# Kernel optimization log

Hardware: AMD Instinct MI355X
Metric: run time of the kernel (lower is better)

## Reference

```python
import jax, jax.numpy as jnp
from jax import lax
import numpy as np

B, C, H, W = 16, 32, 128, 128
R = 8      # region_num
OUT = 32   # out_channels (== in_channels, required by residual add)
K = 3      # kernel_size
PAD = 1    # self.kwargs padding for the correlation conv


def setup_inputs() -> dict:
    key = jax.random.key(0)
    ks = jax.random.split(key, 8)
    n = lambda k, s: jax.random.normal(k, s, dtype=jnp.float32) * 0.05
    return {
        "input": jax.random.normal(ks[0], (B, C, H, W), dtype=jnp.float32),
        "guide_input": jax.random.normal(ks[1], (B, C, H, W), dtype=jnp.float32),
        "w1": n(ks[2], (R * R, C)), "b1": jnp.zeros((R * R,), jnp.float32),
        "w2": n(ks[3], (R, C * OUT, R)), "b2": jnp.zeros((R * C * OUT,), jnp.float32),
        "w_spa": n(ks[4], (R, C)), "b_spa": jnp.zeros((R,), jnp.float32),
        "w_spec": n(ks[5], (R, C)), "b_spec": jnp.zeros((R,), jnp.float32),
        "w_f": n(ks[6], (OUT, 2 * C, 3, 3)), "b_f": jnp.zeros((OUT,), jnp.float32),
    }


def adaptive_avg_pool2d(x, k):
    # torch AdaptiveAvgPool2d bin edges: start=floor(i*H/k), end=ceil((i+1)*H/k)
    Hh, Ww = x.shape[-2], x.shape[-1]
    rows = []
    for i in range(k):
        hs, he = (i * Hh) // k, -(-((i + 1) * Hh) // k)
        cols = []
        for j in range(k):
            ws, we = (j * Ww) // k, -(-((j + 1) * Ww) // k)
            cols.append(x[..., hs:he, ws:we].mean(axis=(-2, -1)))
        rows.append(jnp.stack(cols, axis=-1))
    return jnp.stack(rows, axis=-2)  # [..., k, k]


def asign_index(kernel, guide):
    # kernel: [B, R, OUT, H, W]; guide: [B, R, H, W]
    mask = jax.nn.one_hot(jnp.argmax(guide, axis=1), guide.shape[1], axis=1,
                          dtype=kernel.dtype)  # [B, R, H, W]
    return jnp.sum(kernel * mask[:, :, None], axis=1)  # [B, OUT, H, W]


def reference(input, guide_input, w1, b1, w2, b2, w_spa, b_spa, w_spec, b_spec, w_f, b_f):
    # --- dynamic kernel generation (conv_kernel Sequential) ---
    pooled = adaptive_avg_pool2d(input, K)                                    # [B, C, K, K]
    g = jax.nn.sigmoid(jnp.einsum('bckl,oc->bokl', pooled, w1) + b1[None, :, None, None])  # [B, R*R, K, K]
    g = g.reshape(B, R, R, K, K)
    # grouped 1x1 conv (groups=R): per group in=R, out=C*OUT
    kern = jnp.einsum('brikl,roi->brokl', g, w2).reshape(B, R * C * OUT, K, K)
    kern = kern + b2[None, :, None, None]
    kern = kern.reshape(B, R * OUT, C, K, K)

    # --- correlation: per-sample conv with its own generated kernels (xcorr_fast) ---
    corr = jax.vmap(lambda xi, ki: lax.conv_general_dilated(
        xi[None], ki, (1, 1), [(PAD, PAD), (PAD, PAD)])[0])(input, kern)      # [B, R*OUT, H, W]
    corr = corr.reshape(B, R, OUT, H, W)

    # --- guide features (SpecDynConv / SpecClassifier modeled as 1x1 convs C->R) ---
    gf_spa = jnp.einsum('bchw,rc->brhw', guide_input, w_spa) + b_spa[None, :, None, None]
    gf_spec = jnp.einsum('bchw,rc->brhw', guide_input, w_spec) + b_spec[None, :, None, None]

    # --- argmax one-hot mask select + region-sum ---
    out_spa = asign_index(corr, gf_spa)    # [B, OUT, H, W]
    out_spec = asign_index(corr, gf_spec)  # [B, OUT, H, W]

    # --- fusion conv 3x3 + residual ---
    fused = lax.conv_general_dilated(jnp.concatenate([out_spa, out_spec], axis=1),
                                     w_f, (1, 1), [(1, 1), (1, 1)])
    fused = fused + b_f[None, :, None, None]
    return fused + input
```

## Files before the change

### kernel.cpp

```cpp
#include <hip/hip_runtime.h>
#include <hip/hip_bf16.h>
#include <math.h>

#define Bn 16
#define Cn 32
#define Hn 128
#define Wn 128
#define HW (Hn*Wn)
#define Rn 8
#define OUTn 32
#define PW 130

#define OFF_POOLED 0u
#define OFF_G      18432u
#define OFF_KERNA  55296u
#define OFF_WFA    2414592u
#define OFF_RSEL   2451456u
#define OFF_INTP   3500032u
#define OFF_CATP   20805632u

typedef __attribute__((ext_vector_type(8))) short short8;
typedef __attribute__((ext_vector_type(4))) float floatx4;

static __device__ __forceinline__ unsigned short f2b(float f) {
  __hip_bfloat16 h = __float2bfloat16(f);
  return *reinterpret_cast<unsigned short*>(&h);
}


__global__ __launch_bounds__(64) void pool_kernel(const float* __restrict__ in,
                                                  float* __restrict__ pooled) {
  const int blk = blockIdx.x;
  const int bin = blk % 9, bc = blk / 9;
  const int bi = bin / 3, bj = bin % 3;
  const int s0[3] = {0, 42, 85};
  const int e0[3] = {43, 86, 128};
  const int rs = s0[bi], re = e0[bi];
  const int cs = s0[bj], ce = e0[bj];
  const int n = (re - rs) * (ce - cs);
  const float* img = in + (size_t)bc * HW;
  float acc = 0.f;
  for (int y = rs; y < re; ++y)
    for (int x = cs + (int)threadIdx.x; x < ce; x += 64)
      acc += img[y * Wn + x];
  #pragma unroll
  for (int off = 32; off > 0; off >>= 1) acc += __shfl_down(acc, off, 64);
  if (threadIdx.x == 0) pooled[bc * 9 + bin] = acc / (float)n;
}

__global__ void g_kernel(const float* __restrict__ pooled, const float* __restrict__ w1,
                         const float* __restrict__ b1, float* __restrict__ g) {
  const int idx = blockIdx.x * 256 + threadIdx.x;
  if (idx >= Bn * 64 * 9) return;
  const int bin = idx % 9;
  const int o = (idx / 9) % 64;
  const int b = idx / (9 * 64);
  float acc = b1[o];
  #pragma unroll
  for (int c = 0; c < Cn; ++c)
    acc = fmaf(pooled[(b * Cn + c) * 9 + bin], w1[o * Cn + c], acc);
  g[idx] = 1.f / (1.f + expf(-acc));
}

__global__ void kern_kernel(const float* __restrict__ g, const float* __restrict__ w2,
                            const float* __restrict__ b2, short* __restrict__ kernA) {
  const int idx = blockIdx.x * 256 + threadIdx.x;
  if (idx >= Bn * 8 * 9 * 1024) return;
  const int j  = idx & 7;
  const int m  = (idx >> 3) & 15;
  const int kg = (idx >> 7) & 3;
  const int h  = (idx >> 9) & 1;
  const int t  = (idx >> 10) % 9;
  const int br = idx / 9216;
  const int r = br & 7, b = br >> 3;
  const int c = kg * 8 + j;
  const int u = h * 16 + m;
  const int jidx = u * 32 + c;
  float acc = b2[r * 1024 + jidx];
  #pragma unroll
  for (int i = 0; i < 8; ++i)
    acc = fmaf(g[(b * 64 + r * 8 + i) * 9 + t], w2[(r * 1024 + jidx) * 8 + i], acc);
  kernA[idx] = (short)f2b(acc);
}

__global__ void wf_kernel(const float* __restrict__ w_f, short* __restrict__ wfA) {
  int idx = blockIdx.x * 256 + threadIdx.x;
  if (idx >= 18432) return;
  const int j  = idx & 7;
  const int m  = (idx >> 3) & 15;
  const int kg = (idx >> 7) & 3;
  const int h  = (idx >> 9) & 1;
  const int kb = idx >> 10;
  const int tap = kb >> 1, ch = kb & 1;
  const int ci = ch * 32 + kg * 8 + j;
  const int o = h * 16 + m;
  wfA[idx] = (short)f2b(w_f[(o * 64 + ci) * 9 + tap]);
}


__global__ void halo_kernel(uint4* __restrict__ inTp, uint4* __restrict__ catp) {
  const int idx = blockIdx.x * 256 + threadIdx.x;
  if (idx >= Bn * 520) return;
  const int b = idx / 520, i = idx % 520;
  int y, x;
  if (i < 130)      { y = 0;       x = i; }
  else if (i < 260) { y = 129;     x = i - 130; }
  else if (i < 390) { y = i - 260; x = 0; }
  else              { y = i - 390; x = 129; }
  const size_t pp = (size_t)(b * PW + y) * PW + x;
  const uint4 z = make_uint4(0u, 0u, 0u, 0u);
  #pragma unroll
  for (int q = 0; q < 4; ++q) inTp[pp * 4 + q] = z;
  #pragma unroll
  for (int q = 0; q < 8; ++q) catp[pp * 8 + q] = z;
}


__global__ __launch_bounds__(256) void tr_kernel(const float* __restrict__ in,
                                                 uint4* __restrict__ inTp) {
  __shared__ float lds[32][65];
  const int blk = blockIdx.x;
  const int b = blk >> 8;
  const int p0 = (blk & 255) * 64;
  const int tid = threadIdx.x;
  const int pl = tid & 63;
  const int c0 = tid >> 6;
  #pragma unroll
  for (int cc = 0; cc < 8; ++cc) {
    const int c = cc * 4 + c0;
    lds[c][pl] = in[(size_t)(b * 32 + c) * HW + p0 + pl];
  }
  __syncthreads();
  const int pw = tid >> 2;
  const int cg = (tid & 3) * 8;
  unsigned int w0 = (unsigned)f2b(lds[cg + 0][pw]) | ((unsigned)f2b(lds[cg + 1][pw]) << 16);
  unsigned int w1 = (unsigned)f2b(lds[cg + 2][pw]) | ((unsigned)f2b(lds[cg + 3][pw]) << 16);
  unsigned int w2 = (unsigned)f2b(lds[cg + 4][pw]) | ((unsigned)f2b(lds[cg + 5][pw]) << 16);
  unsigned int w3 = (unsigned)f2b(lds[cg + 6][pw]) | ((unsigned)f2b(lds[cg + 7][pw]) << 16);
  const int p = p0 + pw;
  const int y = p >> 7, x = p & 127;
  const size_t pp = (size_t)(b * PW + y + 1) * PW + (x + 1);
  inTp[pp * 4 + (tid & 3)] = make_uint4(w0, w1, w2, w3);
}


__global__ void rsel_kernel(const float* __restrict__ guide,
                            const float* __restrict__ w_spa, const float* __restrict__ b_spa,
                            const float* __restrict__ w_spec, const float* __restrict__ b_spec,
                            int* __restrict__ rsel) {
  const int idx = blockIdx.x * 256 + threadIdx.x;
  const int b = idx >> 14;
  const int p = idx & (HW - 1);
  float gv[Cn];
  const float* gp = guide + (size_t)b * Cn * HW + p;
  #pragma unroll
  for (int c = 0; c < Cn; ++c) gv[c] = gp[c * HW];
  int best1 = 0, best2 = 0;
  float bv1 = -1e30f, bv2 = -1e30f;
  for (int r = 0; r < Rn; ++r) {
    float v1 = b_spa[r], v2 = b_spec[r];
    #pragma unroll
    for (int c = 0; c < Cn; ++c) {
      v1 = fmaf(gv[c], w_spa[r * Cn + c], v1);
      v2 = fmaf(gv[c], w_spec[r * Cn + c], v2);
    }
    if (v1 > bv1) { bv1 = v1; best1 = r; }
    if (v2 > bv2) { bv2 = v2; best2 = r; }
  }
  rsel[idx] = best1 | (best2 << 8);
}


__global__ __launch_bounds__(256) void stageB_kernel(
    const char* __restrict__ inTp, const short* __restrict__ kernA,
    const int* __restrict__ rsel, char* __restrict__ catp) {
  const int id = blockIdx.x;
  const int chunk = id & 7, r = (id >> 3) & 7, b = id >> 6;
  const int pbase = chunk * 2048;
  __shared__ int lcount;
  __shared__ unsigned short list[4096];
  const int tid = threadIdx.x;
  if (tid == 0) lcount = 0;
  __syncthreads();
  const int* rs = rsel + b * HW + pbase;
  for (int i = tid; i < 2048; i += 256) {
    int v = rs[i];
    if ((v & 255) == r) { int k = atomicAdd(&lcount, 1); list[k] = (unsigned short)i; }
    if ((v >> 8) == r)  { int k = atomicAdd(&lcount, 1); list[k] = (unsigned short)(i | 2048); }
  }
  __syncthreads();
  const int cnt = lcount;
  const int lane = tid & 63, wid = tid >> 6;
  const int l15 = lane & 15, kg = lane >> 4;

  short8 aw[18];
  {
    const short* kb = kernA + (size_t)(b * 8 + r) * 18 * 512;
    #pragma unroll
    for (int f = 0; f < 18; ++f)
      aw[f] = *(const short8*)(kb + f * 512 + kg * 128 + l15 * 8);
  }

  for (int g = wid; g * 16 < cnt; g += 4) {
    const int e16 = g * 16 + l15;
    const bool ev = e16 < cnt;
    const int ent = list[ev ? e16 : 0];
    const int p = pbase + (ent & 2047);
    const int which = ent >> 11;
    const int y = p >> 7, x = p & 127;
    const size_t pp = (size_t)(b * PW + y + 1) * PW + (x + 1);
    const char* base = inTp + pp * 64 + kg * 16;
    floatx4 acc0 = {0.f, 0.f, 0.f, 0.f}, acc1 = {0.f, 0.f, 0.f, 0.f};
    #pragma unroll
    for (int t = 0; t < 9; ++t) {
      const int dy = t / 3 - 1, dx = t % 3 - 1;
      const short8 bx = *(const short8*)(base + (dy * PW + dx) * 64);
      acc0 = __builtin_amdgcn_mfma_f32_16x16x32_bf16(aw[t * 2 + 0], bx, acc0, 0, 0, 0);
      acc1 = __builtin_amdgcn_mfma_f32_16x16x32_bf16(aw[t * 2 + 1], bx, acc1, 0, 0, 0);
    }
    if (ev) {
      char* op = catp + pp * 128 + which * 64 + kg * 8;
      uint2 v0, v1;
      v0.x = (unsigned)f2b(acc0[0]) | ((unsigned)f2b(acc0[1]) << 16);
      v0.y = (unsigned)f2b(acc0[2]) | ((unsigned)f2b(acc0[3]) << 16);
      v1.x = (unsigned)f2b(acc1[0]) | ((unsigned)f2b(acc1[1]) << 16);
      v1.y = (unsigned)f2b(acc1[2]) | ((unsigned)f2b(acc1[3]) << 16);
      *(uint2*)op = v0;
      *(uint2*)(op + 32) = v1;
    }
  }
}


__global__ __launch_bounds__(256, 4) void stageC_kernel(
    const char* __restrict__ catp, const short* __restrict__ wfA,
    const float* __restrict__ b_f, const float* __restrict__ in,
    float* __restrict__ out) {
  __shared__ short lwf[18432];
  const int tid = threadIdx.x;
  {
    const uint4* src = (const uint4*)wfA;
    uint4* dst = (uint4*)lwf;
    #pragma unroll
    for (int i = 0; i < 9; ++i)
      dst[i * 256 + tid] = src[i * 256 + tid];
  }
  __syncthreads();
  const int id = (blockIdx.x & 7) * 128 + (blockIdx.x >> 3);
  const int b = id >> 6, seg = id & 63;
  const int lane = tid & 63, wid = tid >> 6;
  const int l15 = lane & 15, kg = lane >> 4;
  const int pix = seg * 256 + wid * 64 + l15;

  const char* bq[4];
  #pragma unroll
  for (int q = 0; q < 4; ++q) {
    const int p = pix + q * 16;
    const int y = p >> 7, x = p & 127;
    bq[q] = catp + ((size_t)(b * PW + y + 1) * PW + (x + 1)) * 128 + kg * 16;
  }
  floatx4 acc[2][4] = {};
  #pragma unroll
  for (int kb = 0; kb < 18; ++kb) {
    const int tap = kb >> 1, ch = kb & 1;
    const int dy = tap / 3 - 1, dx = tap % 3 - 1;
    const int goff = (dy * PW + dx) * 128 + ch * 64;
    const short8 a0 = *(const short8*)&lwf[(kb * 2 + 0) * 512 + kg * 128 + l15 * 8];
    const short8 a1 = *(const short8*)&lwf[(kb * 2 + 1) * 512 + kg * 128 + l15 * 8];
    #pragma unroll
    for (int q = 0; q < 4; ++q) {
      const short8 bx = *(const short8*)(bq[q] + goff);
      acc[0][q] = __builtin_amdgcn_mfma_f32_16x16x32_bf16(a0, bx, acc[0][q], 0, 0, 0);
      acc[1][q] = __builtin_amdgcn_mfma_f32_16x16x32_bf16(a1, bx, acc[1][q], 0, 0, 0);
    }
  }
  #pragma unroll
  for (int h = 0; h < 2; ++h) {
    const int o0 = h * 16 + kg * 4;
    #pragma unroll
    for (int q = 0; q < 4; ++q) {
      const int p = pix + q * 16;
      #pragma unroll
      for (int reg = 0; reg < 4; ++reg) {
        const size_t oi = (size_t)(b * 32 + o0 + reg) * HW + p;
        out[oi] = acc[h][q][reg] + b_f[o0 + reg] + in[oi];
      }
    }
  }
}


extern "C" void kernel_launch(void* const* d_in, const int* in_sizes, int n_in,
                              void* d_out, int out_size, void* d_ws, size_t ws_size,
                              hipStream_t stream) {
  const float* input  = (const float*)d_in[0];
  const float* guide  = (const float*)d_in[1];
  const float* w1     = (const float*)d_in[2];
  const float* b1     = (const float*)d_in[3];
  const float* w2     = (const float*)d_in[4];
  const float* b2     = (const float*)d_in[5];
  const float* w_spa  = (const float*)d_in[6];
  const float* b_spa  = (const float*)d_in[7];
  const float* w_spec = (const float*)d_in[8];
  const float* b_spec = (const float*)d_in[9];
  const float* w_f    = (const float*)d_in[10];
  const float* b_f    = (const float*)d_in[11];
  float* out = (float*)d_out;

  char* ws = (char*)d_ws;
  float* pooled = (float*)(ws + OFF_POOLED);
  float* g      = (float*)(ws + OFF_G);
  short* kernA  = (short*)(ws + OFF_KERNA);
  short* wfA    = (short*)(ws + OFF_WFA);
  int*   rsel   = (int*)(ws + OFF_RSEL);
  uint4* inTp   = (uint4*)(ws + OFF_INTP);
  char*  catp   = (char*)(ws + OFF_CATP);

  pool_kernel<<<Bn * Cn * 9, 64, 0, stream>>>(input, pooled);
  g_kernel<<<(Bn * 64 * 9 + 255) / 256, 256, 0, stream>>>(pooled, w1, b1, g);
  kern_kernel<<<Bn * 8 * 9 * 1024 / 256, 256, 0, stream>>>(g, w2, b2, kernA);
  wf_kernel<<<72, 256, 0, stream>>>(w_f, wfA);
  halo_kernel<<<(Bn * 520 + 255) / 256, 256, 0, stream>>>(inTp, (uint4*)catp);
  tr_kernel<<<Bn * 256, 256, 0, stream>>>(input, inTp);
  rsel_kernel<<<Bn * HW / 256, 256, 0, stream>>>(guide, w_spa, b_spa, w_spec, b_spec, rsel);
  stageB_kernel<<<1024, 256, 0, stream>>>((const char*)inTp, kernA, rsel, catp);
  stageC_kernel<<<1024, 256, 0, stream>>>(catp, wfA, b_f, input, out);
}
```

Measured before the change: 252.5 us.

## Fuse adaptive pooling into transpose kernel and software-pipeline MFMA loads

Removes the separate pool_kernel by accumulating adaptive-pool bin sums with atomics inside the transpose kernel, which already holds the input tile in LDS. The sums are zeroed in halo_kernel and normalized in g_kernel. This saves a full extra read of the input and one launch. Separately, stageB now hoists all nine tap loads before its MFMAs, and stageC double-buffers tap loads so the next tap's loads are issued while the current tap's MFMAs run. The costs are atomic contention on a few addresses, float-atomic nondeterminism in the pooled sums, and higher register pressure in the pipelined loops.

```diff
diff --git a/kernel.cpp b/kernel.cpp
--- a/kernel.cpp
+++ b/kernel.cpp
@@ -28,37 +28,20 @@
 }
 
 
-__global__ __launch_bounds__(64) void pool_kernel(const float* __restrict__ in,
-                                                  float* __restrict__ pooled) {
-  const int blk = blockIdx.x;
-  const int bin = blk % 9, bc = blk / 9;
-  const int bi = bin / 3, bj = bin % 3;
-  const int s0[3] = {0, 42, 85};
-  const int e0[3] = {43, 86, 128};
-  const int rs = s0[bi], re = e0[bi];
-  const int cs = s0[bj], ce = e0[bj];
-  const int n = (re - rs) * (ce - cs);
-  const float* img = in + (size_t)bc * HW;
-  float acc = 0.f;
-  for (int y = rs; y < re; ++y)
-    for (int x = cs + (int)threadIdx.x; x < ce; x += 64)
-      acc += img[y * Wn + x];
-  #pragma unroll
-  for (int off = 32; off > 0; off >>= 1) acc += __shfl_down(acc, off, 64);
-  if (threadIdx.x == 0) pooled[bc * 9 + bin] = acc / (float)n;
-}
-
-__global__ void g_kernel(const float* __restrict__ pooled, const float* __restrict__ w1,
+__global__ void g_kernel(const float* __restrict__ poolsum, const float* __restrict__ w1,
                          const float* __restrict__ b1, float* __restrict__ g) {
   const int idx = blockIdx.x * 256 + threadIdx.x;
   if (idx >= Bn * 64 * 9) return;
   const int bin = idx % 9;
   const int o = (idx / 9) % 64;
   const int b = idx / (9 * 64);
+  const int bi = bin / 3, bj = bin % 3;
+  const float szr[3] = {43.f, 44.f, 43.f};
+  const float invn = 1.f / (szr[bi] * szr[bj]);
   float acc = b1[o];
   #pragma unroll
   for (int c = 0; c < Cn; ++c)
-    acc = fmaf(pooled[(b * Cn + c) * 9 + bin], w1[o * Cn + c], acc);
+    acc = fmaf(poolsum[(b * Cn + c) * 9 + bin] * invn, w1[o * Cn + c], acc);
   g[idx] = 1.f / (1.f + expf(-acc));
 }
 
@@ -98,8 +81,10 @@
 }
 
 
-__global__ void halo_kernel(uint4* __restrict__ inTp, uint4* __restrict__ catp) {
+__global__ void halo_kernel(uint4* __restrict__ inTp, uint4* __restrict__ catp,
+                            float* __restrict__ poolsum) {
   const int idx = blockIdx.x * 256 + threadIdx.x;
+  if (idx < Bn * Cn * 9) poolsum[idx] = 0.f;
   if (idx >= Bn * 520) return;
   const int b = idx / 520, i = idx % 520;
   int y, x;
@@ -117,7 +102,8 @@
 
 
 __global__ __launch_bounds__(256) void tr_kernel(const float* __restrict__ in,
-                                                 uint4* __restrict__ inTp) {
+                                                 uint4* __restrict__ inTp,
+                                                 float* __restrict__ poolsum) {
   __shared__ float lds[32][65];
   const int blk = blockIdx.x;
   const int b = blk >> 8;
@@ -131,16 +117,46 @@
     lds[c][pl] = in[(size_t)(b * 32 + c) * HW + p0 + pl];
   }
   __syncthreads();
-  const int pw = tid >> 2;
-  const int cg = (tid & 3) * 8;
-  unsigned int w0 = (unsigned)f2b(lds[cg + 0][pw]) | ((unsigned)f2b(lds[cg + 1][pw]) << 16);
-  unsigned int w1 = (unsigned)f2b(lds[cg + 2][pw]) | ((unsigned)f2b(lds[cg + 3][pw]) << 16);
-  unsigned int w2 = (unsigned)f2b(lds[cg + 4][pw]) | ((unsigned)f2b(lds[cg + 5][pw]) << 16);
-  unsigned int w3 = (unsigned)f2b(lds[cg + 6][pw]) | ((unsigned)f2b(lds[cg + 7][pw]) << 16);
-  const int p = p0 + pw;
-  const int y = p >> 7, x = p & 127;
-  const size_t pp = (size_t)(b * PW + y + 1) * PW + (x + 1);
-  inTp[pp * 4 + (tid & 3)] = make_uint4(w0, w1, w2, w3);
+  {
+    const int pw = tid >> 2;
+    const int cg = (tid & 3) * 8;
+    unsigned int w0 = (unsigned)f2b(lds[cg + 0][pw]) | ((unsigned)f2b(lds[cg + 1][pw]) << 16);
+    unsigned int w1 = (unsigned)f2b(lds[cg + 2][pw]) | ((unsigned)f2b(lds[cg + 3][pw]) << 16);
+    unsigned int w2 = (unsigned)f2b(lds[cg + 4][pw]) | ((unsigned)f2b(lds[cg + 5][pw]) << 16);
+    unsigned int w3 = (unsigned)f2b(lds[cg + 6][pw]) | ((unsigned)f2b(lds[cg + 7][pw]) << 16);
+    const int p = p0 + pw;
+    const int y = p >> 7, x = p & 127;
+    const size_t pp = (size_t)(b * PW + y + 1) * PW + (x + 1);
+    inTp[pp * 4 + (tid & 3)] = make_uint4(w0, w1, w2, w3);
+  }
+  const int x0 = p0 & 127;
+  const int y  = p0 >> 7;
+  const int c  = tid >> 3, j = tid & 7;
+  const int plo = j * 8;
+  const int splitA = x0 ? 22 : 43;
+  const int splitB = x0 ? 21 : 42;
+  float sumA = 0.f, sumB = 0.f;
+  #pragma unroll
+  for (int k = 0; k < 8; ++k) {
+    const float v = lds[c][plo + k];
+    if (plo + k < splitA)  sumA += v;
+    if (plo + k >= splitB) sumB += v;
+  }
+  sumA += __shfl_down(sumA, 4, 64); sumB += __shfl_down(sumB, 4, 64);
+  sumA += __shfl_down(sumA, 2, 64); sumB += __shfl_down(sumB, 2, 64);
+  sumA += __shfl_down(sumA, 1, 64); sumB += __shfl_down(sumB, 1, 64);
+  if (j == 0) {
+    const int bi0 = (y < 43) ? 0 : ((y < 86) ? 1 : 2);
+    const int bi1 = (y == 42) ? 1 : ((y == 85) ? 2 : -1);
+    const int bjA = x0 ? 1 : 0, bjB = x0 ? 2 : 1;
+    float* ps = poolsum + (b * Cn + c) * 9;
+    atomicAdd(ps + bi0 * 3 + bjA, sumA);
+    atomicAdd(ps + bi0 * 3 + bjB, sumB);
+    if (bi1 >= 0) {
+      atomicAdd(ps + bi1 * 3 + bjA, sumA);
+      atomicAdd(ps + bi1 * 3 + bjB, sumB);
+    }
+  }
 }
 
 
@@ -171,7 +187,7 @@
 }
 
 
-__global__ __launch_bounds__(256) void stageB_kernel(
+__global__ void stageB_kernel(
     const char* __restrict__ inTp, const short* __restrict__ kernA,
     const int* __restrict__ rsel, char* __restrict__ catp) {
   const int id = blockIdx.x;
@@ -210,13 +226,17 @@
     const int y = p >> 7, x = p & 127;
     const size_t pp = (size_t)(b * PW + y + 1) * PW + (x + 1);
     const char* base = inTp + pp * 64 + kg * 16;
-    floatx4 acc0 = {0.f, 0.f, 0.f, 0.f}, acc1 = {0.f, 0.f, 0.f, 0.f};
+    short8 bx[9];
     #pragma unroll
     for (int t = 0; t < 9; ++t) {
       const int dy = t / 3 - 1, dx = t % 3 - 1;
-      const short8 bx = *(const short8*)(base + (dy * PW + dx) * 64);
-      acc0 = __builtin_amdgcn_mfma_f32_16x16x32_bf16(aw[t * 2 + 0], bx, acc0, 0, 0, 0);
-      acc1 = __builtin_amdgcn_mfma_f32_16x16x32_bf16(aw[t * 2 + 1], bx, acc1, 0, 0, 0);
+      bx[t] = *(const short8*)(base + (dy * PW + dx) * 64);
+    }
+    floatx4 acc0 = {0.f, 0.f, 0.f, 0.f}, acc1 = {0.f, 0.f, 0.f, 0.f};
+    #pragma unroll
+    for (int t = 0; t < 9; ++t) {
+      acc0 = __builtin_amdgcn_mfma_f32_16x16x32_bf16(aw[t * 2 + 0], bx[t], acc0, 0, 0, 0);
+      acc1 = __builtin_amdgcn_mfma_f32_16x16x32_bf16(aw[t * 2 + 1], bx[t], acc1, 0, 0, 0);
     }
     if (ev) {
       char* op = catp + pp * 128 + which * 64 + kg * 8;
@@ -260,20 +280,44 @@
     bq[q] = catp + ((size_t)(b * PW + y + 1) * PW + (x + 1)) * 128 + kg * 16;
   }
   floatx4 acc[2][4] = {};
-  #pragma unroll
-  for (int kb = 0; kb < 18; ++kb) {
-    const int tap = kb >> 1, ch = kb & 1;
-    const int dy = tap / 3 - 1, dx = tap % 3 - 1;
-    const int goff = (dy * PW + dx) * 128 + ch * 64;
-    const short8 a0 = *(const short8*)&lwf[(kb * 2 + 0) * 512 + kg * 128 + l15 * 8];
-    const short8 a1 = *(const short8*)&lwf[(kb * 2 + 1) * 512 + kg * 128 + l15 * 8];
-    #pragma unroll
-    for (int q = 0; q < 4; ++q) {
-      const short8 bx = *(const short8*)(bq[q] + goff);
-      acc[0][q] = __builtin_amdgcn_mfma_f32_16x16x32_bf16(a0, bx, acc[0][q], 0, 0, 0);
-      acc[1][q] = __builtin_amdgcn_mfma_f32_16x16x32_bf16(a1, bx, acc[1][q], 0, 0, 0);
-    }
-  }
+  short8 bxA[8], bxB[8];
+
+#define GOFF(T) (((((T) / 3) - 1) * PW + (((T) % 3) - 1)) * 128)
+
+#define LOADTAP(BUF, T)                                              \
+  { _Pragma("unroll")                                                \
+    for (int q = 0; q < 4; ++q) {                                    \
+      BUF[q * 2 + 0] = *(const short8*)(bq[q] + GOFF(T));            \
+      BUF[q * 2 + 1] = *(const short8*)(bq[q] + GOFF(T) + 64);       \
+    } }
+
+#define MFMATAP(BUF, T)                                                              \
+  { const short8 a00 = *(const short8*)&lwf[(4*(T)+0)*512 + kg*128 + l15*8];          \
+    const short8 a01 = *(const short8*)&lwf[(4*(T)+1)*512 + kg*128 + l15*8];          \
+    const short8 a10 = *(const short8*)&lwf[(4*(T)+2)*512 + kg*128 + l15*8];          \
+    const short8 a11 = *(const short8*)&lwf[(4*(T)+3)*512 + kg*128 + l15*8];          \
+    _Pragma("unroll")                                                                 \
+    for (int q = 0; q < 4; ++q) {                                                     \
+      acc[0][q] = __builtin_amdgcn_mfma_f32_16x16x32_bf16(a00, BUF[q*2+0], acc[0][q], 0, 0, 0); \
+      acc[1][q] = __builtin_amdgcn_mfma_f32_16x16x32_bf16(a01, BUF[q*2+0], acc[1][q], 0, 0, 0); \
+      acc[0][q] = __builtin_amdgcn_mfma_f32_16x16x32_bf16(a10, BUF[q*2+1], acc[0][q], 0, 0, 0); \
+      acc[1][q] = __builtin_amdgcn_mfma_f32_16x16x32_bf16(a11, BUF[q*2+1], acc[1][q], 0, 0, 0); \
+    } }
+
+  LOADTAP(bxA, 0)
+  LOADTAP(bxB, 1)  MFMATAP(bxA, 0)
+  LOADTAP(bxA, 2)  MFMATAP(bxB, 1)
+  LOADTAP(bxB, 3)  MFMATAP(bxA, 2)
+  LOADTAP(bxA, 4)  MFMATAP(bxB, 3)
+  LOADTAP(bxB, 5)  MFMATAP(bxA, 4)
+  LOADTAP(bxA, 6)  MFMATAP(bxB, 5)
+  LOADTAP(bxB, 7)  MFMATAP(bxA, 6)
+  LOADTAP(bxA, 8)  MFMATAP(bxB, 7)
+                   MFMATAP(bxA, 8)
+#undef LOADTAP
+#undef MFMATAP
+#undef GOFF
+
   #pragma unroll
   for (int h = 0; h < 2; ++h) {
     const int o0 = h * 16 + kg * 4;
@@ -308,7 +352,7 @@
   float* out = (float*)d_out;
 
   char* ws = (char*)d_ws;
-  float* pooled = (float*)(ws + OFF_POOLED);
+  float* poolsum = (float*)(ws + OFF_POOLED);
   float* g      = (float*)(ws + OFF_G);
   short* kernA  = (short*)(ws + OFF_KERNA);
   short* wfA    = (short*)(ws + OFF_WFA);
@@ -316,12 +360,11 @@
   uint4* inTp   = (uint4*)(ws + OFF_INTP);
   char*  catp   = (char*)(ws + OFF_CATP);
 
-  pool_kernel<<<Bn * Cn * 9, 64, 0, stream>>>(input, pooled);
-  g_kernel<<<(Bn * 64 * 9 + 255) / 256, 256, 0, stream>>>(pooled, w1, b1, g);
+  wf_kernel<<<72, 256, 0, stream>>>(w_f, wfA);
+  halo_kernel<<<(Bn * 520 + 255) / 256, 256, 0, stream>>>(inTp, (uint4*)catp, poolsum);
+  tr_kernel<<<Bn * 256, 256, 0, stream>>>(input, inTp, poolsum);
+  g_kernel<<<(Bn * 64 * 9 + 255) / 256, 256, 0, stream>>>(poolsum, w1, b1, g);
   kern_kernel<<<Bn * 8 * 9 * 1024 / 256, 256, 0, stream>>>(g, w2, b2, kernA);
-  wf_kernel<<<72, 256, 0, stream>>>(w_f, wfA);
-  halo_kernel<<<(Bn * 520 + 255) / 256, 256, 0, stream>>>(inTp, (uint4*)catp);
-  tr_kernel<<<Bn * 256, 256, 0, stream>>>(input, inTp);
   rsel_kernel<<<Bn * HW / 256, 256, 0, stream>>>(guide, w_spa, b_spa, w_spec, b_spec, rsel);
   stageB_kernel<<<1024, 256, 0, stream>>>((const char*)inTp, kernA, rsel, catp);
   stageC_kernel<<<1024, 256, 0, stream>>>(catp, wfA, b_f, input, out);
```

After: 265.3 us. +5.1%, slower.
